# Performance work log

Hardware: AMD Instinct MI355X
Metric: run time of the kernel (lower is better)

Reference implementation:

```python
import jax, jax.numpy as jnp
import numpy as np

D_H, D_G, D_PROJ = 1280, 768, 256
SCALE = D_PROJ ** (-0.5)

def setup_inputs() -> dict:
    key = jax.random.key(0)
    k1, k2, k3, k4 = jax.random.split(key, 4)
    B, L, T = 8, 4096, 512
    H = jax.random.normal(k1, (B, L, D_H), dtype=jnp.float32)
    G = jax.random.normal(k2, (B, T, D_G), dtype=jnp.float32)
    attn_mask = jnp.zeros((B, L), dtype=bool)  # True = pad/ignore
    # nn.Linear weights: (out_features, in_features)
    Wk = jax.random.normal(k3, (D_PROJ, D_H), dtype=jnp.float32) * (D_H ** -0.5)
    Wq = jax.random.normal(k4, (D_PROJ, D_G), dtype=jnp.float32) * (D_G ** -0.5)
    return {"H": H, "G": G, "attn_mask": attn_mask, "Wk": Wk, "Wq": Wq}

def reference(H, G, attn_mask, Wk, Wq):
    # K = Wk(H): (B,L,P); Q = Wq(G): (B,T,P)
    K = jnp.einsum('bld,pd->blp', H, Wk)
    Q = jnp.einsum('btd,pd->btp', G, Wq)
    # scores (B,T,L); streaming two-pass softmax in the original is exactly
    # softmax over L -> compute it stably in one fused expression here.
    logits = jnp.einsum('btp,blp->btl', Q, K) * SCALE
    logits = jnp.where(attn_mask[:, None, :], -jnp.inf, logits)
    alpha = jax.nn.softmax(logits, axis=-1)
    Z = jnp.einsum('btl,bld->btd', alpha, H)  # (B,T,Dh)
    return Z
```

## Files before the change

### kernel.cpp

```cpp
#include <hip/hip_runtime.h>
#include <hip/hip_bf16.h>
#include <stdint.h>


typedef float f32x4 __attribute__((ext_vector_type(4)));
typedef short bf16x8 __attribute__((ext_vector_type(8)));

__device__ __forceinline__ unsigned short f2bf(float f) {
    __hip_bfloat16 h = __float2bfloat16(f);
    return __builtin_bit_cast(unsigned short, h);
}
__device__ __forceinline__ float bf2f(unsigned short h) {
    union { uint32_t u; float f; } v; v.u = ((uint32_t)h) << 16;
    return v.f;
}

__device__ __forceinline__ int xcdswz(int bx, int nbx) {
    int cpx = nbx >> 3;
    return (bx & 7) * cpx + (bx >> 3);
}

__device__ __forceinline__ int lidx(int row, int kshort) {
    return row * 40 + (((kshort >> 3) ^ ((row >> 3) & 3)) << 3) + (kshort & 7);
}

template<bool AF32, bool BF32, bool OBF16, bool TNF>
__global__ __launch_bounds__(256)
void gemm_bt(const void* __restrict__ Ap, const void* __restrict__ Bp,
             void* __restrict__ Cp, int M, int N, int K,
             long sA, long sB, long sC, float scale)
{
    __shared__ __align__(16) unsigned short lA[128 * 40];
    __shared__ __align__(16) unsigned short lB[128 * 40];

    const int bx = xcdswz(blockIdx.x, gridDim.x);
    const int mt = M >> 7, nt = N >> 7;
    const int tm = TNF ? (bx / nt) : (bx % mt);
    const int tn = TNF ? (bx % nt) : (bx / mt);
    const int b  = blockIdx.y;
    const int tid = threadIdx.x;
    const int lane = tid & 63, wv = tid >> 6;
    const int wr = wv >> 1, wc = wv & 1;
    const int fr = lane & 15, fk = lane >> 4;

    f32x4 acc[4][4] = {};

    const char* Abase = (const char*)Ap;
    const char* Bbase = (const char*)Bp;

    for (int k0 = 0; k0 < K; k0 += 32) {
        if constexpr (AF32) {
            const float* A = (const float*)Abase + (long)b * sA + (long)tm * 128 * K + k0;
            #pragma unroll
            for (int it = 0; it < 4; ++it) {
                int chunk = it * 256 + tid;
                int row = chunk >> 3;
                int kc  = (chunk & 7) << 2;
                const float4 v = *(const float4*)(A + (long)row * K + kc);
                ushort4 w;
                w.x = f2bf(v.x); w.y = f2bf(v.y); w.z = f2bf(v.z); w.w = f2bf(v.w);
                *(ushort4*)(&lA[lidx(row, kc)]) = w;
            }
        } else {
            const unsigned short* A = (const unsigned short*)Abase + (long)b * sA + (long)tm * 128 * K + k0;
            #pragma unroll
            for (int it = 0; it < 2; ++it) {
                int chunk = it * 256 + tid;
                int row = chunk >> 2;
                int kc  = (chunk & 3) << 3;
                *(uint4*)(&lA[lidx(row, kc)]) = *(const uint4*)(A + (long)row * K + kc);
            }
        }
        if constexpr (BF32) {
            const float* B = (const float*)Bbase + (long)b * sB + (long)tn * 128 * K + k0;
            #pragma unroll
            for (int it = 0; it < 4; ++it) {
                int chunk = it * 256 + tid;
                int row = chunk >> 3;
                int kc  = (chunk & 7) << 2;
                const float4 v = *(const float4*)(B + (long)row * K + kc);
                ushort4 w;
                w.x = f2bf(v.x); w.y = f2bf(v.y); w.z = f2bf(v.z); w.w = f2bf(v.w);
                *(ushort4*)(&lB[lidx(row, kc)]) = w;
            }
        } else {
            const unsigned short* B = (const unsigned short*)Bbase + (long)b * sB + (long)tn * 128 * K + k0;
            #pragma unroll
            for (int it = 0; it < 2; ++it) {
                int chunk = it * 256 + tid;
                int row = chunk >> 2;
                int kc  = (chunk & 3) << 3;
                *(uint4*)(&lB[lidx(row, kc)]) = *(const uint4*)(B + (long)row * K + kc);
            }
        }
        __syncthreads();
        bf16x8 af[4], bfr[4];
        #pragma unroll
        for (int i = 0; i < 4; ++i)
            af[i] = *(const bf16x8*)(&lA[lidx(wr * 64 + i * 16 + fr, fk * 8)]);
        #pragma unroll
        for (int i = 0; i < 4; ++i)
            bfr[i] = *(const bf16x8*)(&lB[lidx(wc * 64 + i * 16 + fr, fk * 8)]);
        #pragma unroll
        for (int mi = 0; mi < 4; ++mi)
            #pragma unroll
            for (int ni = 0; ni < 4; ++ni)
                acc[mi][ni] = __builtin_amdgcn_mfma_f32_16x16x32_bf16(af[mi], bfr[ni], acc[mi][ni], 0, 0, 0);
        __syncthreads();
    }

    if constexpr (OBF16) {
        unsigned short* C = (unsigned short*)Cp + (long)b * sC + ((long)tm * 128) * N + (long)tn * 128;
        #pragma unroll
        for (int mi = 0; mi < 4; ++mi)
            #pragma unroll
            for (int ni = 0; ni < 4; ++ni)
                #pragma unroll
                for (int j = 0; j < 4; ++j) {
                    int m = wr * 64 + mi * 16 + fk * 4 + j;
                    int n = wc * 64 + ni * 16 + fr;
                    C[(long)m * N + n] = f2bf(acc[mi][ni][j] * scale);
                }
    } else {
        float* C = (float*)Cp + (long)b * sC + ((long)tm * 128) * N + (long)tn * 128;
        #pragma unroll
        for (int mi = 0; mi < 4; ++mi)
            #pragma unroll
            for (int ni = 0; ni < 4; ++ni)
                #pragma unroll
                for (int j = 0; j < 4; ++j) {
                    int m = wr * 64 + mi * 16 + fk * 4 + j;
                    int n = wc * 64 + ni * 16 + fr;
                    C[(long)m * N + n] = acc[mi][ni][j] * scale;
                }
    }
}

__global__ __launch_bounds__(256)
void gemm_kn(const unsigned short* __restrict__ Ap, const float* __restrict__ Bp,
             float* __restrict__ Cp, int M, int N, int K,
             long sA, long sB, long sC)
{
    __shared__ __align__(16) unsigned short lA[128 * 40];
    __shared__ __align__(16) unsigned short lB[64 * 40];

    const int bx = xcdswz(blockIdx.x, gridDim.x);
    const int mt = M >> 7;
    const int tm = bx % mt;
    const int tn = bx / mt;
    const int b  = blockIdx.y;
    const int tid = threadIdx.x;
    const int lane = tid & 63, wv = tid >> 6;
    const int wr = wv >> 1, wc = wv & 1;
    const int fr = lane & 15, fk = lane >> 4;

    f32x4 acc[4][2] = {};

    const unsigned short* A0 = Ap + (long)b * sA + (long)tm * 128 * K;
    const int nn    = tid & 63;
    const int khalf = tid >> 6;

    for (int k0 = 0; k0 < K; k0 += 32) {
        #pragma unroll
        for (int it = 0; it < 2; ++it) {
            int chunk = it * 256 + tid;
            int row = chunk >> 2;
            int kc  = (chunk & 3) << 3;
            *(uint4*)(&lA[lidx(row, kc)]) = *(const uint4*)(A0 + (long)row * K + k0 + kc);
        }
        {
            const float* Bb = Bp + (long)b * sB + (long)(k0 + khalf * 8) * N + (long)tn * 64 + nn;
            unsigned short t8[8];
            #pragma unroll
            for (int kk = 0; kk < 8; ++kk)
                t8[kk] = f2bf(Bb[(long)kk * N]);
            *(uint4*)(&lB[lidx(nn, khalf * 8)]) = *(uint4*)(&t8[0]);
        }
        __syncthreads();
        bf16x8 af[4], bfr[2];
        #pragma unroll
        for (int i = 0; i < 4; ++i)
            af[i] = *(const bf16x8*)(&lA[lidx(wr * 64 + i * 16 + fr, fk * 8)]);
        #pragma unroll
        for (int i = 0; i < 2; ++i)
            bfr[i] = *(const bf16x8*)(&lB[lidx(wc * 32 + i * 16 + fr, fk * 8)]);
        #pragma unroll
        for (int mi = 0; mi < 4; ++mi)
            #pragma unroll
            for (int ni = 0; ni < 2; ++ni)
                acc[mi][ni] = __builtin_amdgcn_mfma_f32_16x16x32_bf16(af[mi], bfr[ni], acc[mi][ni], 0, 0, 0);
        __syncthreads();
    }

    float* C = Cp + (long)b * sC + ((long)tm * 128) * N + (long)tn * 64;
    #pragma unroll
    for (int mi = 0; mi < 4; ++mi)
        #pragma unroll
        for (int ni = 0; ni < 2; ++ni)
            #pragma unroll
            for (int j = 0; j < 4; ++j) {
                int m = wr * 64 + mi * 16 + fk * 4 + j;
                int n = wc * 32 + ni * 16 + fr;
                C[(long)m * N + n] = acc[mi][ni][j];
            }
}

__global__ __launch_bounds__(256)
void softmax_rows(unsigned short* __restrict__ S, const unsigned char* __restrict__ mask)
{
    const int row = blockIdx.x;
    const int b = row >> 9;
    const long base = (long)row * 4096;
    const int tid = threadIdx.x, lane = tid & 63, wv = tid >> 6;
    __shared__ float red[8];

    uint4 s0 = *(const uint4*)(S + base + tid * 16);
    uint4 s1 = *(const uint4*)(S + base + tid * 16 + 8);
    uint4 mv = *(const uint4*)(mask + (long)b * 4096 + tid * 16);
    const unsigned char* mb = (const unsigned char*)&mv;

    unsigned int words[8] = { s0.x, s0.y, s0.z, s0.w, s1.x, s1.y, s1.z, s1.w };
    float x[16];
    #pragma unroll
    for (int i = 0; i < 8; ++i) {
        x[2 * i]     = bf2f((unsigned short)(words[i] & 0xffffu));
        x[2 * i + 1] = bf2f((unsigned short)(words[i] >> 16));
    }
    #pragma unroll
    for (int i = 0; i < 16; ++i)
        if (mb[i]) x[i] = -1e30f;

    float m = x[0];
    #pragma unroll
    for (int i = 1; i < 16; ++i) m = fmaxf(m, x[i]);
    #pragma unroll
    for (int off = 32; off; off >>= 1) m = fmaxf(m, __shfl_xor(m, off));
    if (lane == 0) red[wv] = m;
    __syncthreads();
    m = fmaxf(fmaxf(red[0], red[1]), fmaxf(red[2], red[3]));

    float p[16];
    float s = 0.f;
    #pragma unroll
    for (int i = 0; i < 16; ++i) { p[i] = __expf(x[i] - m); s += p[i]; }
    #pragma unroll
    for (int off = 32; off; off >>= 1) s += __shfl_xor(s, off);
    if (lane == 0) red[4 + wv] = s;
    __syncthreads();
    s = (red[4] + red[5]) + (red[6] + red[7]);
    const float inv = 1.0f / s;

    unsigned int ow[8];
    #pragma unroll
    for (int i = 0; i < 8; ++i) {
        unsigned int lo = f2bf(p[2 * i] * inv);
        unsigned int hi = f2bf(p[2 * i + 1] * inv);
        ow[i] = lo | (hi << 16);
    }
    uint4 o0 = { ow[0], ow[1], ow[2], ow[3] };
    uint4 o1 = { ow[4], ow[5], ow[6], ow[7] };
    *(uint4*)(S + base + tid * 16)     = o0;
    *(uint4*)(S + base + tid * 16 + 8) = o1;
}

extern "C" void kernel_launch(void* const* d_in, const int* in_sizes, int n_in,
                              void* d_out, int out_size, void* d_ws, size_t ws_size,
                              hipStream_t stream)
{
    const float*         H    = (const float*)d_in[0];
    const float*         G    = (const float*)d_in[1];
    const unsigned char* mask = (const unsigned char*)d_in[2];
    const float*         Wk   = (const float*)d_in[3];
    const float*         Wq   = (const float*)d_in[4];
    float*               out  = (float*)d_out;

    unsigned short* Kb = (unsigned short*)d_ws;
    unsigned short* Qb = Kb + (long)8 * 4096 * 256;
    unsigned short* Sb = Qb + (long)8 * 512 * 256;

    gemm_bt<true, true, true, true><<<dim3(512, 1), 256, 0, stream>>>(
        H, Wk, Kb, 32768, 256, 1280, 0, 0, 0, 1.0f);
    gemm_bt<true, true, true, true><<<dim3(64, 1), 256, 0, stream>>>(
        G, Wq, Qb, 4096, 256, 768, 0, 0, 0, 1.0f);
    gemm_bt<false, false, true, false><<<dim3(128, 8), 256, 0, stream>>>(
        Qb, Kb, Sb, 512, 4096, 256,
        (long)512 * 256, (long)4096 * 256, (long)512 * 4096, 0.0625f);
    softmax_rows<<<dim3(4096), 256, 0, stream>>>(Sb, mask);
    gemm_kn<<<dim3(80, 8), 256, 0, stream>>>(
        Sb, H, out, 512, 1280, 4096,
        (long)512 * 4096, (long)4096 * 1280, (long)512 * 1280);
}
```

Baseline: 243.5 us.

## Pre-transpose H to bf16 and use direct-to-LDS loads for bf16 GEMMs

Result: slower. 279.7 us (+14.9%).

```diff
diff --git a/kernel.cpp b/kernel.cpp
--- a/kernel.cpp
+++ b/kernel.cpp
@@ -18,6 +18,13 @@
 __device__ __forceinline__ int xcdswz(int bx, int nbx) {
     int cpx = nbx >> 3;
     return (bx & 7) * cpx + (bx >> 3);
+}
+
+__device__ __forceinline__ void gload16(const unsigned short* g, unsigned short* l) {
+    __builtin_amdgcn_global_load_lds(
+        (const __attribute__((address_space(1))) void*)g,
+        (__attribute__((address_space(3))) void*)l,
+        16, 0, 0);
 }
 
 __device__ __forceinline__ int lidx(int row, int kshort) {
@@ -136,6 +143,126 @@
     }
 }
 
+template<int TN, bool OBF16>
+__global__ __launch_bounds__(256)
+void gemm_bt16(const unsigned short* __restrict__ Ap, const unsigned short* __restrict__ Bp,
+               void* __restrict__ Cp, int M, int N, int K,
+               long sA, long sB, long sC, float scale)
+{
+    constexpr int NB = TN / 32;
+    constexpr int BISS = TN / 64;
+    __shared__ __align__(16) unsigned short lA[128 * 32];
+    __shared__ __align__(16) unsigned short lB[TN * 32];
+
+    const int bx = xcdswz(blockIdx.x, gridDim.x);
+    const int mt = M >> 7;
+    const int tm = bx % mt, tn = bx / mt;
+    const int b  = blockIdx.y;
+    const int tid = threadIdx.x;
+    const int lane = tid & 63, wv = tid >> 6;
+    const int wr = wv >> 1, wc = wv & 1;
+    const int fr = lane & 15, fk = lane >> 4;
+
+    f32x4 acc[4][NB] = {};
+
+    const unsigned short* A0 = Ap + (long)b * sA + (long)tm * 128 * K;
+    const unsigned short* B0 = Bp + (long)b * sB + (long)tn * TN * K;
+
+    for (int k0 = 0; k0 < K; k0 += 32) {
+        #pragma unroll
+        for (int q = 0; q < 2; ++q) {
+            int slot = wv * 128 + q * 64 + lane;
+            int row = slot >> 2, kc = (slot & 3) << 3;
+            gload16(A0 + (long)row * K + k0 + kc, lA + (size_t)(wv * 128 + q * 64) * 8);
+        }
+        #pragma unroll
+        for (int q = 0; q < BISS; ++q) {
+            int slot = wv * (BISS * 64) + q * 64 + lane;
+            int row = slot >> 2, kc = (slot & 3) << 3;
+            gload16(B0 + (long)row * K + k0 + kc, lB + (size_t)(wv * (BISS * 64) + q * 64) * 8);
+        }
+        __syncthreads();
+        bf16x8 af[4], bfv[NB];
+        #pragma unroll
+        for (int i = 0; i < 4; ++i)
+            af[i] = *(const bf16x8*)(lA + (wr * 64 + i * 16 + fr) * 32 + fk * 8);
+        #pragma unroll
+        for (int i = 0; i < NB; ++i)
+            bfv[i] = *(const bf16x8*)(lB + (wc * (TN / 2) + i * 16 + fr) * 32 + fk * 8);
+        #pragma unroll
+        for (int mi = 0; mi < 4; ++mi)
+            #pragma unroll
+            for (int ni = 0; ni < NB; ++ni)
+                acc[mi][ni] = __builtin_amdgcn_mfma_f32_16x16x32_bf16(af[mi], bfv[ni], acc[mi][ni], 0, 0, 0);
+        __syncthreads();
+    }
+
+    if constexpr (OBF16) {
+        unsigned short* C = (unsigned short*)Cp + (long)b * sC + ((long)tm * 128) * N + (long)tn * TN;
+        #pragma unroll
+        for (int mi = 0; mi < 4; ++mi)
+            #pragma unroll
+            for (int ni = 0; ni < NB; ++ni)
+                #pragma unroll
+                for (int j = 0; j < 4; ++j) {
+                    int m = wr * 64 + mi * 16 + fk * 4 + j;
+                    int n = wc * (TN / 2) + ni * 16 + fr;
+                    C[(long)m * N + n] = f2bf(acc[mi][ni][j] * scale);
+                }
+    } else {
+        float* C = (float*)Cp + (long)b * sC + ((long)tm * 128) * N + (long)tn * TN;
+        #pragma unroll
+        for (int mi = 0; mi < 4; ++mi)
+            #pragma unroll
+            for (int ni = 0; ni < NB; ++ni)
+                #pragma unroll
+                for (int j = 0; j < 4; ++j) {
+                    int m = wr * 64 + mi * 16 + fk * 4 + j;
+                    int n = wc * (TN / 2) + ni * 16 + fr;
+                    C[(long)m * N + n] = acc[mi][ni][j] * scale;
+                }
+    }
+}
+
+__global__ __launch_bounds__(256)
+void transpose_h(const float* __restrict__ H, unsigned short* __restrict__ Hbt)
+{
+    __shared__ unsigned short lT[64 * 72];
+    const int ntile = 64 * 20 * 8;
+    for (int tileid = blockIdx.x; tileid < ntile; tileid += gridDim.x) {
+        int tmp = tileid;
+        const int dt = tmp % 20; tmp /= 20;
+        const int lt = tmp % 64;
+        const int b  = tmp / 64;
+        const int l0 = lt * 64, d0 = dt * 64;
+        const float* Hs = H + ((long)b * 4096 + l0) * 1280 + d0;
+        #pragma unroll
+        for (int it = 0; it < 4; ++it) {
+            int chunk = it * 256 + threadIdx.x;
+            int lr = chunk >> 4, dc4 = (chunk & 15) << 2;
+            float4 v = *(const float4*)(Hs + (long)lr * 1280 + dc4);
+            unsigned short w[4] = { f2bf(v.x), f2bf(v.y), f2bf(v.z), f2bf(v.w) };
+            #pragma unroll
+            for (int j = 0; j < 4; ++j) {
+                int d = dc4 + j;
+                int sl = (lr & 15) | ((((lr >> 4) ^ (d >> 2)) & 3) << 4);
+                lT[d * 72 + sl] = w[j];
+            }
+        }
+        __syncthreads();
+        {
+            int drow = threadIdx.x >> 2, lc = threadIdx.x & 3;
+            int slc = lc ^ ((drow >> 2) & 3);
+            const uint4* src = (const uint4*)(lT + drow * 72 + slc * 16);
+            unsigned short* dst = Hbt + ((long)b * 1280 + d0 + drow) * 4096 + l0 + lc * 16;
+            uint4 v0 = src[0], v1 = src[1];
+            *(uint4*)(dst)     = v0;
+            *(uint4*)(dst + 8) = v1;
+        }
+        __syncthreads();
+    }
+}
+
 __global__ __launch_bounds__(256)
 void gemm_kn(const unsigned short* __restrict__ Ap, const float* __restrict__ Bp,
              float* __restrict__ Cp, int M, int N, int K,
@@ -274,19 +401,38 @@
     const float*         Wq   = (const float*)d_in[4];
     float*               out  = (float*)d_out;
 
-    unsigned short* Kb = (unsigned short*)d_ws;
-    unsigned short* Qb = Kb + (long)8 * 4096 * 256;
-    unsigned short* Sb = Qb + (long)8 * 512 * 256;
+    const long nK = (long)8 * 4096 * 256;
+    const long nQ = (long)8 * 512 * 256;
+    const long nS = (long)8 * 512 * 4096;
+    const long nH = (long)8 * 1280 * 4096;
+
+    unsigned short* Kb  = (unsigned short*)d_ws;
+    unsigned short* Qb  = Kb + nK;
+    unsigned short* Sb  = Qb + nQ;
+    unsigned short* Hbt = Sb + nS;
+    const bool big = ws_size >= (size_t)(nK + nQ + nS + nH) * 2;
 
     gemm_bt<true, true, true, true><<<dim3(512, 1), 256, 0, stream>>>(
         H, Wk, Kb, 32768, 256, 1280, 0, 0, 0, 1.0f);
     gemm_bt<true, true, true, true><<<dim3(64, 1), 256, 0, stream>>>(
         G, Wq, Qb, 4096, 256, 768, 0, 0, 0, 1.0f);
-    gemm_bt<false, false, true, false><<<dim3(128, 8), 256, 0, stream>>>(
-        Qb, Kb, Sb, 512, 4096, 256,
-        (long)512 * 256, (long)4096 * 256, (long)512 * 4096, 0.0625f);
-    softmax_rows<<<dim3(4096), 256, 0, stream>>>(Sb, mask);
-    gemm_kn<<<dim3(80, 8), 256, 0, stream>>>(
-        Sb, H, out, 512, 1280, 4096,
-        (long)512 * 4096, (long)4096 * 1280, (long)512 * 1280);
-}
+
+    if (big) {
+        transpose_h<<<dim3(2048), 256, 0, stream>>>(H, Hbt);
+        gemm_bt16<128, true><<<dim3(128, 8), 256, 0, stream>>>(
+            Qb, Kb, Sb, 512, 4096, 256,
+            (long)512 * 256, (long)4096 * 256, (long)512 * 4096, 0.0625f);
+        softmax_rows<<<dim3(4096), 256, 0, stream>>>(Sb, mask);
+        gemm_bt16<64, false><<<dim3(80, 8), 256, 0, stream>>>(
+            Sb, Hbt, out, 512, 1280, 4096,
+            (long)512 * 4096, (long)1280 * 4096, (long)512 * 1280, 1.0f);
+    } else {
+        gemm_bt<false, false, true, false><<<dim3(128, 8), 256, 0, stream>>>(
+            Qb, Kb, Sb, 512, 4096, 256,
+            (long)512 * 256, (long)4096 * 256, (long)512 * 4096, 0.0625f);
+        softmax_rows<<<dim3(4096), 256, 0, stream>>>(Sb, mask);
+        gemm_kn<<<dim3(80, 8), 256, 0, stream>>>(
+            Sb, H, out, 512, 1280, 4096,
+            (long)512 * 4096, (long)4096 * 1280, (long)512 * 1280);
+    }
+}
```

## Emit transposed bf16 H in projection and use direct-to-LDS bf16 GEMMs

Applied to the files above, without the earlier changes.

New measurement: 282.3 us. 1.16x slower.

```diff
diff --git a/kernel.cpp b/kernel.cpp
--- a/kernel.cpp
+++ b/kernel.cpp
@@ -20,24 +20,30 @@
     return (bx & 7) * cpx + (bx >> 3);
 }
 
+__device__ __forceinline__ void gload16(const unsigned short* g, unsigned short* l) {
+    __builtin_amdgcn_global_load_lds(
+        (const __attribute__((address_space(1))) void*)g,
+        (__attribute__((address_space(3))) void*)l,
+        16, 0, 0);
+}
+
 __device__ __forceinline__ int lidx(int row, int kshort) {
     return row * 40 + (((kshort >> 3) ^ ((row >> 3) & 3)) << 3) + (kshort & 7);
 }
 
-template<bool AF32, bool BF32, bool OBF16, bool TNF>
+template<bool WRITE_HBT>
 __global__ __launch_bounds__(256)
-void gemm_bt(const void* __restrict__ Ap, const void* __restrict__ Bp,
-             void* __restrict__ Cp, int M, int N, int K,
-             long sA, long sB, long sC, float scale)
+void gemm_proj(const float* __restrict__ Ap, const float* __restrict__ Bp,
+               unsigned short* __restrict__ Cp, int M, int N, int K,
+               unsigned short* __restrict__ Hbt)
 {
     __shared__ __align__(16) unsigned short lA[128 * 40];
     __shared__ __align__(16) unsigned short lB[128 * 40];
 
     const int bx = xcdswz(blockIdx.x, gridDim.x);
-    const int mt = M >> 7, nt = N >> 7;
-    const int tm = TNF ? (bx / nt) : (bx % mt);
-    const int tn = TNF ? (bx % nt) : (bx / mt);
-    const int b  = blockIdx.y;
+    const int nt = N >> 7;
+    const int tm = bx / nt;
+    const int tn = bx % nt;
     const int tid = threadIdx.x;
     const int lane = tid & 63, wv = tid >> 6;
     const int wr = wv >> 1, wc = wv & 1;
@@ -45,12 +51,9 @@
 
     f32x4 acc[4][4] = {};
 
-    const char* Abase = (const char*)Ap;
-    const char* Bbase = (const char*)Bp;
-
     for (int k0 = 0; k0 < K; k0 += 32) {
-        if constexpr (AF32) {
-            const float* A = (const float*)Abase + (long)b * sA + (long)tm * 128 * K + k0;
+        {
+            const float* A = Ap + (long)tm * 128 * K + k0;
             #pragma unroll
             for (int it = 0; it < 4; ++it) {
                 int chunk = it * 256 + tid;
@@ -60,19 +63,20 @@
                 ushort4 w;
                 w.x = f2bf(v.x); w.y = f2bf(v.y); w.z = f2bf(v.z); w.w = f2bf(v.w);
                 *(ushort4*)(&lA[lidx(row, kc)]) = w;
-            }
-        } else {
-            const unsigned short* A = (const unsigned short*)Abase + (long)b * sA + (long)tm * 128 * K + k0;
-            #pragma unroll
-            for (int it = 0; it < 2; ++it) {
-                int chunk = it * 256 + tid;
-                int row = chunk >> 2;
-                int kc  = (chunk & 3) << 3;
-                *(uint4*)(&lA[lidx(row, kc)]) = *(const uint4*)(A + (long)row * K + kc);
-            }
-        }
-        if constexpr (BF32) {
-            const float* B = (const float*)Bbase + (long)b * sB + (long)tn * 128 * K + k0;
+                if constexpr (WRITE_HBT) {
+                    if (tn == 0) {
+                        int gm = tm * 128 + row;
+                        int bb = gm >> 12, ll = gm & 4095;
+                        unsigned short wa[4] = { w.x, w.y, w.z, w.w };
+                        #pragma unroll
+                        for (int j = 0; j < 4; ++j)
+                            Hbt[((long)bb * 1280 + k0 + kc + j) * 4096 + ll] = wa[j];
+                    }
+                }
+            }
+        }
+        {
+            const float* B = Bp + (long)tn * 128 * K + k0;
             #pragma unroll
             for (int it = 0; it < 4; ++it) {
                 int chunk = it * 256 + tid;
@@ -83,15 +87,6 @@
                 w.x = f2bf(v.x); w.y = f2bf(v.y); w.z = f2bf(v.z); w.w = f2bf(v.w);
                 *(ushort4*)(&lB[lidx(row, kc)]) = w;
             }
-        } else {
-            const unsigned short* B = (const unsigned short*)Bbase + (long)b * sB + (long)tn * 128 * K + k0;
-            #pragma unroll
-            for (int it = 0; it < 2; ++it) {
-                int chunk = it * 256 + tid;
-                int row = chunk >> 2;
-                int kc  = (chunk & 3) << 3;
-                *(uint4*)(&lB[lidx(row, kc)]) = *(const uint4*)(B + (long)row * K + kc);
-            }
         }
         __syncthreads();
         bf16x8 af[4], bfr[4];
@@ -109,7 +104,85 @@
         __syncthreads();
     }
 
-    if constexpr (OBF16) {
+    unsigned short* C = Cp + ((long)tm * 128) * N + (long)tn * 128;
+    #pragma unroll
+    for (int mi = 0; mi < 4; ++mi)
+        #pragma unroll
+        for (int ni = 0; ni < 4; ++ni)
+            #pragma unroll
+            for (int j = 0; j < 4; ++j) {
+                int m = wr * 64 + mi * 16 + fk * 4 + j;
+                int n = wc * 64 + ni * 16 + fr;
+                C[(long)m * N + n] = f2bf(acc[mi][ni][j]);
+            }
+}
+
+template<bool OF32>
+__global__ __launch_bounds__(256)
+void gemm_bt16s(const unsigned short* __restrict__ Ap, const unsigned short* __restrict__ Bp,
+                void* __restrict__ Cp, int M, int N, int K,
+                long sA, long sB, long sC, float scale)
+{
+    __shared__ __align__(16) unsigned short lA[128 * 64];
+    __shared__ __align__(16) unsigned short lB[128 * 64];
+
+    const int bx = xcdswz(blockIdx.x, gridDim.x);
+    const int nt = N >> 7;
+    const int tm = bx / nt, tn = bx % nt;
+    const int b  = blockIdx.y;
+    const int tid = threadIdx.x;
+    const int lane = tid & 63, wv = tid >> 6;
+    const int wr = wv >> 1, wc = wv & 1;
+    const int fr = lane & 15, fk = lane >> 4;
+
+    f32x4 acc[4][4] = {};
+
+    const unsigned short* A0 = Ap + (long)b * sA + (long)tm * 128 * K;
+    const unsigned short* B0 = Bp + (long)b * sB + (long)tn * 128 * K;
+
+    for (int k0 = 0; k0 < K; k0 += 64) {
+        #pragma unroll
+        for (int q = 0; q < 4; ++q) {
+            int slot = wv * 256 + q * 64 + lane;
+            int row = slot >> 3, c = slot & 7;
+            int ks = (c ^ (row & 7)) << 3;
+            gload16(A0 + (long)row * K + k0 + ks, lA + (size_t)(wv * 256 + q * 64) * 8);
+            gload16(B0 + (long)row * K + k0 + ks, lB + (size_t)(wv * 256 + q * 64) * 8);
+        }
+        __syncthreads();
+        bf16x8 af[2][4], bfv[2][4];
+        #pragma unroll
+        for (int ks = 0; ks < 2; ++ks) {
+            int csw = ((ks * 4 + fk) ^ (fr & 7)) << 3;
+            #pragma unroll
+            for (int i = 0; i < 4; ++i) {
+                af[ks][i]  = *(const bf16x8*)(lA + (wr * 64 + i * 16 + fr) * 64 + csw);
+                bfv[ks][i] = *(const bf16x8*)(lB + (wc * 64 + i * 16 + fr) * 64 + csw);
+            }
+        }
+        #pragma unroll
+        for (int mi = 0; mi < 4; ++mi)
+            #pragma unroll
+            for (int ni = 0; ni < 4; ++ni)
+                #pragma unroll
+                for (int ks = 0; ks < 2; ++ks)
+                    acc[mi][ni] = __builtin_amdgcn_mfma_f32_16x16x32_bf16(af[ks][mi], bfv[ks][ni], acc[mi][ni], 0, 0, 0);
+        __syncthreads();
+    }
+
+    if constexpr (OF32) {
+        float* C = (float*)Cp + (long)b * sC + ((long)tm * 128) * N + (long)tn * 128;
+        #pragma unroll
+        for (int mi = 0; mi < 4; ++mi)
+            #pragma unroll
+            for (int ni = 0; ni < 4; ++ni)
+                #pragma unroll
+                for (int j = 0; j < 4; ++j) {
+                    int m = wr * 64 + mi * 16 + fk * 4 + j;
+                    int n = wc * 64 + ni * 16 + fr;
+                    C[(long)m * N + n] = acc[mi][ni][j] * scale;
+                }
+    } else {
         unsigned short* C = (unsigned short*)Cp + (long)b * sC + ((long)tm * 128) * N + (long)tn * 128;
         #pragma unroll
         for (int mi = 0; mi < 4; ++mi)
@@ -120,18 +193,6 @@
                     int m = wr * 64 + mi * 16 + fk * 4 + j;
                     int n = wc * 64 + ni * 16 + fr;
                     C[(long)m * N + n] = f2bf(acc[mi][ni][j] * scale);
-                }
-    } else {
-        float* C = (float*)Cp + (long)b * sC + ((long)tm * 128) * N + (long)tn * 128;
-        #pragma unroll
-        for (int mi = 0; mi < 4; ++mi)
-            #pragma unroll
-            for (int ni = 0; ni < 4; ++ni)
-                #pragma unroll
-                for (int j = 0; j < 4; ++j) {
-                    int m = wr * 64 + mi * 16 + fk * 4 + j;
-                    int n = wc * 64 + ni * 16 + fr;
-                    C[(long)m * N + n] = acc[mi][ni][j] * scale;
                 }
     }
 }
@@ -274,19 +335,40 @@
     const float*         Wq   = (const float*)d_in[4];
     float*               out  = (float*)d_out;
 
-    unsigned short* Kb = (unsigned short*)d_ws;
-    unsigned short* Qb = Kb + (long)8 * 4096 * 256;
-    unsigned short* Sb = Qb + (long)8 * 512 * 256;
-
-    gemm_bt<true, true, true, true><<<dim3(512, 1), 256, 0, stream>>>(
-        H, Wk, Kb, 32768, 256, 1280, 0, 0, 0, 1.0f);
-    gemm_bt<true, true, true, true><<<dim3(64, 1), 256, 0, stream>>>(
-        G, Wq, Qb, 4096, 256, 768, 0, 0, 0, 1.0f);
-    gemm_bt<false, false, true, false><<<dim3(128, 8), 256, 0, stream>>>(
-        Qb, Kb, Sb, 512, 4096, 256,
-        (long)512 * 256, (long)4096 * 256, (long)512 * 4096, 0.0625f);
-    softmax_rows<<<dim3(4096), 256, 0, stream>>>(Sb, mask);
-    gemm_kn<<<dim3(80, 8), 256, 0, stream>>>(
-        Sb, H, out, 512, 1280, 4096,
-        (long)512 * 4096, (long)4096 * 1280, (long)512 * 1280);
-}
+    const long nK = (long)8 * 4096 * 256;
+    const long nQ = (long)8 * 512 * 256;
+    const long nS = (long)8 * 512 * 4096;
+    const long nH = (long)8 * 1280 * 4096;
+
+    unsigned short* Kb  = (unsigned short*)d_ws;
+    unsigned short* Qb  = Kb + nK;
+    unsigned short* Sb  = Qb + nQ;
+    unsigned short* Hbt = Sb + nS;
+    const bool big = ws_size >= (size_t)(nK + nQ + nS + nH) * 2;
+
+    if (big) {
+        gemm_proj<true><<<dim3(512, 1), 256, 0, stream>>>(
+            H, Wk, Kb, 32768, 256, 1280, Hbt);
+        gemm_proj<false><<<dim3(64, 1), 256, 0, stream>>>(
+            G, Wq, Qb, 4096, 256, 768, nullptr);
+        gemm_bt16s<false><<<dim3(128, 8), 256, 0, stream>>>(
+            Qb, Kb, Sb, 512, 4096, 256,
+            (long)512 * 256, (long)4096 * 256, (long)512 * 4096, 0.0625f);
+        softmax_rows<<<dim3(4096), 256, 0, stream>>>(Sb, mask);
+        gemm_bt16s<true><<<dim3(40, 8), 256, 0, stream>>>(
+            Sb, Hbt, out, 512, 1280, 4096,
+            (long)512 * 4096, (long)1280 * 4096, (long)512 * 1280, 1.0f);
+    } else {
+        gemm_proj<false><<<dim3(512, 1), 256, 0, stream>>>(
+            H, Wk, Kb, 32768, 256, 1280, nullptr);
+        gemm_proj<false><<<dim3(64, 1), 256, 0, stream>>>(
+            G, Wq, Qb, 4096, 256, 768, nullptr);
+        gemm_bt16s<false><<<dim3(128, 8), 256, 0, stream>>>(
+            Qb, Kb, Sb, 512, 4096, 256,
+            (long)512 * 256, (long)4096 * 256, (long)512 * 4096, 0.0625f);
+        softmax_rows<<<dim3(4096), 256, 0, stream>>>(Sb, mask);
+        gemm_kn<<<dim3(80, 8), 256, 0, stream>>>(
+            Sb, H, out, 512, 1280, 4096,
+            (long)512 * 4096, (long)4096 * 1280, (long)512 * 1280);
+    }
+}
```
